# Kernel optimization log

Measured on AMD Instinct MI355X. Metric: run time of the kernel, lower is better.

The kernel has to match this reference:

```python
import jax, jax.numpy as jnp
import numpy as np

GROUPS = 32
EPS = 1e-5


def group_norm(x, gamma, beta):
    # x: [B,H,W,C], channels_last, groups over channel dim (Keras GroupNormalization default)
    B, H, W, C = x.shape
    xg = x.reshape(B, H, W, GROUPS, C // GROUPS)
    mean = xg.mean(axis=(1, 2, 4), keepdims=True)
    var = xg.var(axis=(1, 2, 4), keepdims=True)
    xn = ((xg - mean) * jax.lax.rsqrt(var + EPS)).reshape(B, H, W, C)
    return xn * gamma + beta


def conv1x1(x, w, b):
    # 1x1 conv == per-pixel dense: [B,H,W,C] x [C,D] -> [B,H,W,D]
    return jnp.einsum('bhwc,cd->bhwd', x, w) + b


def setup_inputs() -> dict:
    key = jax.random.key(0)
    ks = jax.random.split(key, 10)
    C = 512
    s = 1.0 / np.sqrt(C)
    inp = {
        'x': jax.random.normal(ks[0], (2, 64, 64, C), dtype=jnp.float32),
        'gamma': jnp.ones((C,), jnp.float32),
        'beta': jnp.zeros((C,), jnp.float32),
        'wq': jax.random.normal(ks[1], (C, C), jnp.float32) * s,
        'bq': jnp.zeros((C,), jnp.float32),
        'wk': jax.random.normal(ks[2], (C, C), jnp.float32) * s,
        'bk': jnp.zeros((C,), jnp.float32),
        'wv': jax.random.normal(ks[3], (C, C), jnp.float32) * s,
        'bv': jnp.zeros((C,), jnp.float32),
        'wp': jax.random.normal(ks[4], (C, C), jnp.float32) * s,
        'bp': jnp.zeros((C,), jnp.float32),
    }
    return inp


def reference(x, gamma, beta, wq, bq, wk, bk, wv, bv, wp, bp):
    B, H, W, C = x.shape
    N = H * W
    xn = group_norm(x, gamma, beta)
    q = conv1x1(xn, wq, bq).reshape(B, N, C)
    k = conv1x1(xn, wk, bk).reshape(B, N, C)
    v = conv1x1(xn, wv, bv).reshape(B, N, C)
    scale = 1.0 / jnp.sqrt(jnp.asarray(C, x.dtype))
    scores = jnp.einsum('bnc,bmc->bnm', q, k) * scale  # [B,N,N]
    attn = jax.nn.softmax(scores, axis=-1)
    out = jnp.einsum('bnm,bmc->bnc', attn, v).reshape(B, H, W, C)
    return conv1x1(out, wp, bp) + x
```

## Files before the change

kernel.cpp:

```cpp
#include <hip/hip_runtime.h>
#include <hip/hip_fp16.h>

typedef _Float16 half_t;
typedef _Float16 half8 __attribute__((ext_vector_type(8)));
typedef float floatx4 __attribute__((ext_vector_type(4)));

static constexpr int BATCH = 2;
static constexpr int NSP = 4096;
static constexpr int CH = 512;
static constexpr int NQKV = 3 * CH;
static constexpr int KSPLIT = 4;

static constexpr size_t OFF_STATS = 0;
static constexpr size_t OFF_ROWSUM = 512;
static constexpr size_t OFF_PST = 33280;
static constexpr size_t OFF_WQKV = 196608;
static constexpr size_t WQKV_BYTES = (size_t)NQKV * CH * 2;
static constexpr size_t OFF_WP = OFF_WQKV + WQKV_BYTES;
static constexpr size_t WP_BYTES = (size_t)CH * CH * 2;
static constexpr size_t OFF_XN = OFF_WP + WP_BYTES;
static constexpr size_t XN_BYTES = (size_t)BATCH * NSP * CH * 2;
static constexpr size_t OFF_QKV = OFF_XN + XN_BYTES;
static constexpr size_t QKV_BYTES = (size_t)BATCH * NSP * NQKV * 2;
static constexpr size_t OFF_VT = OFF_QKV + QKV_BYTES;
static constexpr size_t OFF_AO = OFF_VT + XN_BYTES;
static constexpr size_t OFF_S = OFF_AO + XN_BYTES;
static constexpr size_t S_BYTES_1 = (size_t)NSP * NSP * 2;
static constexpr size_t OFF_PART = OFF_XN;

__device__ __forceinline__ void gld16(void* lds, const void* g) {
  __builtin_amdgcn_global_load_lds(
      (__attribute__((address_space(1))) void*)(g),
      (__attribute__((address_space(3))) void*)(lds),
      16, 0, 0);
}

#define VMCNT(n) asm volatile("s_waitcnt vmcnt(" #n ")" ::: "memory")
#define LGKM0()                                         \
  do {                                                  \
    asm volatile("s_waitcnt lgkmcnt(0)" ::: "memory");  \
    __builtin_amdgcn_sched_barrier(0);                  \
  } while (0)

__global__ __launch_bounds__(256) void prep(
    const float* __restrict__ x, float* __restrict__ pst,
    const float* __restrict__ w0, const float* __restrict__ w1,
    const float* __restrict__ w2, const float* __restrict__ w3,
    half_t* __restrict__ o0, half_t* __restrict__ o1,
    half_t* __restrict__ o2, half_t* __restrict__ o3) {
  __shared__ float gs[32], gs2[32];
  __shared__ float tw[32][33];
  const int bid = (int)blockIdx.x;
  const int tid = (int)threadIdx.x;
  if (bid < 512) {
    const int b = bid >> 8;
    const int chunk = bid & 255;
    int g = ((tid * 4) & (CH - 1)) >> 4;
    const float* base = x + (long)b * NSP * CH + (long)chunk * 16 * CH + tid * 4;
    float s = 0.f, s2 = 0.f;
#pragma unroll
    for (int it = 0; it < 8; ++it) {
      floatx4 v = *(const floatx4*)(base + (long)it * 1024);
#pragma unroll
      for (int r = 0; r < 4; ++r) { s += v[r]; s2 += v[r] * v[r]; }
    }
    if (tid < 32) { gs[tid] = 0.f; gs2[tid] = 0.f; }
    __syncthreads();
    atomicAdd(&gs[g], s);
    atomicAdd(&gs2[g], s2);
    __syncthreads();
    if (tid < 32) {
      long idx = ((long)(b * 256 + chunk) * 32 + tid) * 2;
      pst[idx] = gs[tid];
      pst[idx + 1] = gs2[tid];
    }
  } else {
    const int t = bid - 512;
    const int wz = t >> 8;
    const int r = t & 255;
    const float* w; half_t* o;
    switch (wz) {
      case 0: w = w0; o = o0; break;
      case 1: w = w1; o = o1; break;
      case 2: w = w2; o = o2; break;
      default: w = w3; o = o3; break;
    }
    int d0 = (r & 15) * 32, c0 = (r >> 4) * 32;
    int tx = tid & 31, ty = tid >> 5;
#pragma unroll
    for (int i = 0; i < 4; ++i)
      tw[ty + i * 8][tx] = w[(long)(c0 + ty + i * 8) * CH + d0 + tx];
    __syncthreads();
#pragma unroll
    for (int i = 0; i < 4; ++i) {
      int d = ty + i * 8;
      o[(long)(d0 + d) * CH + c0 + tx] = (half_t)tw[tx][d];
    }
  }
}

__global__ __launch_bounds__(256) void gn_finalize(const float* __restrict__ pst,
                                                   float* __restrict__ st,
                                                   float* __restrict__ rowsum) {
  int tid = (int)threadIdx.x;
  int bg = tid & 63;
  int p = tid >> 6;
  int b = bg >> 5, g = bg & 31;
  float s = 0.f, s2 = 0.f;
  for (int j = 0; j < 64; ++j) {
    int chunk = p * 64 + j;
    long idx = ((long)(b * 256 + chunk) * 32 + g) * 2;
    s += pst[idx];
    s2 += pst[idx + 1];
  }
  __shared__ float rs[64][4], rs2[64][4];
  rs[bg][p] = s;
  rs2[bg][p] = s2;
  __syncthreads();
  if (tid < 64) {
    float ts = rs[tid][0] + rs[tid][1] + rs[tid][2] + rs[tid][3];
    float ts2 = rs2[tid][0] + rs2[tid][1] + rs2[tid][2] + rs2[tid][3];
    const float inv = 1.f / 65536.f;
    float mean = ts * inv;
    float var = ts2 * inv - mean * mean;
    st[tid * 2] = mean;
    st[tid * 2 + 1] = rsqrtf(var + 1e-5f);
  }
  floatx4* rz = (floatx4*)rowsum;
#pragma unroll
  for (int j = 0; j < 8; ++j)
    rz[tid + j * 256] = floatx4{0.f, 0.f, 0.f, 0.f};
}

__global__ __launch_bounds__(256) void gn_apply(const float* __restrict__ x,
                                                const float* __restrict__ st,
                                                const float* __restrict__ gamma,
                                                const float* __restrict__ beta,
                                                half_t* __restrict__ xn) {
  long i = ((long)blockIdx.x * 256 + threadIdx.x) * 8;
  int c = (int)(i & (CH - 1));
  int b = (int)(i >> 21);
  int g = c >> 4;
  float mean = st[((b << 5) + g) * 2];
  float rstd = st[((b << 5) + g) * 2 + 1];
  floatx4 a = *(const floatx4*)(x + i);
  floatx4 d = *(const floatx4*)(x + i + 4);
  half8 o;
#pragma unroll
  for (int r = 0; r < 4; ++r) {
    o[r]     = (half_t)((a[r] - mean) * rstd * gamma[c + r] + beta[c + r]);
    o[r + 4] = (half_t)((d[r] - mean) * rstd * gamma[c + r + 4] + beta[c + r + 4]);
  }
  *(half8*)(xn + i) = o;
}

__global__ __launch_bounds__(256) void transpose_v(const half_t* __restrict__ v,
                                                   half_t* __restrict__ vt) {
  __shared__ half_t t[32][33];
  int b = blockIdx.z;
  int d0 = blockIdx.x * 32, n0 = blockIdx.y * 32;
  int tx = threadIdx.x & 31, ty = threadIdx.x >> 5;
  const half_t* vb = v + (long)b * NSP * NQKV;
  half_t* ob = vt + (long)b * NSP * CH;
#pragma unroll
  for (int i = 0; i < 4; ++i)
    t[ty + i * 8][tx] = vb[(long)(n0 + ty + i * 8) * NQKV + d0 + tx];
  __syncthreads();
#pragma unroll
  for (int i = 0; i < 4; ++i) {
    int d = ty + i * 8;
    ob[(long)(d0 + d) * NSP + n0 + tx] = t[tx][d];
  }
}

template <int BM, int BN, int BK, int EPI, int SWZ, int KSP, typename OutT>
__global__ __launch_bounds__(256) void gemm_nt(
    const half_t* __restrict__ X, const half_t* __restrict__ Y,
    OutT* __restrict__ Co, const float* __restrict__ b0,
    const float* __restrict__ b1, const float* __restrict__ b2,
    const float* __restrict__ resid, float* __restrict__ rowsum,
    int M, int N, int K, int ldx, int ldy, int ldc,
    long xbs, long ybs, long cbs, float scale) {
  constexpr int SM = BM / 32;
  constexpr int SN = BN / 32;
  constexpr int ROWS = BM + BN;
  constexpr int CPR = BK / 8;
  constexpr int RPW = 64 / CPR;
  constexpr int ROUNDS = (ROWS * BK * 2) / 4096;
  constexpr int KSTEPS = BK / 32;
  static_assert(BM % (4 * RPW) == 0, "no As/Bs straddle within a round");
  __shared__ __align__(16) half_t Sh[ROWS * BK];

  const int zb = blockIdx.z / KSP;
  const int ks = blockIdx.z % KSP;
  int bx, by;
  if (SWZ == 1) {
    int lin = (int)(blockIdx.x + gridDim.x * blockIdx.y);
    int wmt = 256 / (int)gridDim.x;
    by = wmt * (lin >> 8) + ((lin & 255) % wmt);
    bx = (lin & 255) / wmt;
  } else if (SWZ == 2) {
    by = blockIdx.x;
    bx = blockIdx.y;
  } else {
    bx = blockIdx.x;
    by = blockIdx.y;
  }

  const half_t* Xb = X + (long)zb * xbs + (long)ks * K;
  const half_t* Yb = Y + (long)zb * ybs + (long)ks * K;
  OutT* Cb = Co + (long)blockIdx.z * cbs;

  const int m0 = by * BM;
  const int n0 = bx * BN;
  const int tid = (int)threadIdx.x;
  const int wave = tid >> 6;
  const int lane = tid & 63;
  const int quad = lane >> 4;
  const int l16 = lane & 15;
  const int wm = wave >> 1;
  const int wn = wave & 1;

  floatx4 acc[SM][SN] = {};

  const int srow = lane / CPR;
  const int schunk = lane % CPR;
  const char* Xc = (const char*)Xb;

  int soff[ROUNDS];
  int xoff[ROUNDS];
  float xinv[ROUNDS];
#pragma unroll
  for (int r = 0; r < ROUNDS; ++r) {
    int row = r * (4 * RPW) + wave * RPW + srow;
    int gchunk = schunk ^ (row & (CPR - 1));
    const char* p = (row < BM)
        ? (const char*)(Xb + (long)(m0 + row) * ldx)
        : (const char*)(Yb + (long)(n0 + row - BM) * ldy);
    soff[r] = (int)(p + gchunk * 16 - Xc);
    if (EPI == 4) {
      if (row < BM) {
        int m = m0 + row;
        int zbm = m >> 12;
        int inner = m & (NSP - 1);
        xoff[r] = zbm * (KSPLIT * NSP * CH) + inner * CH + gchunk * 8;
        xinv[r] = 1.f / rowsum[m];
      } else {
        xoff[r] = 0;
        xinv[r] = 0.f;
      }
    }
  }

  int offA[SM], offB[SN];
#pragma unroll
  for (int i = 0; i < SM; ++i) {
    int m = wm * (BM / 2) + i * 16 + l16;
    int cc = quad ^ (m & (CPR - 1));
    offA[i] = (m * BK + cc * 8) * 2;
  }
#pragma unroll
  for (int j = 0; j < SN; ++j) {
    int n = wn * (BN / 2) + j * 16 + l16;
    int cc = quad ^ (n & (CPR - 1));
    offB[j] = (BM * BK + n * BK + cc * 8) * 2;
  }

  for (int k0 = 0; k0 < K; k0 += BK) {
#pragma unroll
    for (int r = 0; r < ROUNDS; ++r) {
      int row = r * (4 * RPW) + wave * RPW + srow;
      if (EPI == 4 && row < BM) continue;
      gld16((char*)Sh + (r * 4 + wave) * 1024, Xc + (long)soff[r]);
      soff[r] += BK * 2;
    }
    if (EPI == 4) {
#pragma unroll
      for (int r = 0; r < ROUNDS; ++r) {
        int row = r * (4 * RPW) + wave * RPW + srow;
        if (row >= BM) continue;
        const half_t* pp = X + xoff[r];
        float s[8] = {};
#pragma unroll
        for (int s4 = 0; s4 < KSPLIT; ++s4) {
          half8 h = *(const half8*)(pp + (long)s4 * (NSP * (long)CH));
#pragma unroll
          for (int e = 0; e < 8; ++e) s[e] += (float)h[e];
        }
        half8 o;
#pragma unroll
        for (int e = 0; e < 8; ++e) o[e] = (half_t)(s[e] * xinv[r]);
        *(half8*)((char*)Sh + (r * 4 + wave) * 1024 + lane * 16) = o;
        xoff[r] += BK;
      }
    }
    __syncthreads();

#pragma unroll
    for (int kk = 0; kk < KSTEPS; ++kk) {
      const int kx = kk << 6;
      half8 af[SM], bf[SN];
#pragma unroll
      for (int i = 0; i < SM; ++i)
        af[i] = *(const half8*)((const char*)Sh + (offA[i] ^ kx));
#pragma unroll
      for (int j = 0; j < SN; ++j)
        bf[j] = *(const half8*)((const char*)Sh + (offB[j] ^ kx));
#pragma unroll
      for (int i = 0; i < SM; ++i)
#pragma unroll
        for (int j = 0; j < SN; ++j)
          acc[i][j] = __builtin_amdgcn_mfma_f32_16x16x32_f16(af[i], bf[j], acc[i][j], 0, 0, 0);
    }
    __syncthreads();
  }

#pragma unroll
  for (int i = 0; i < SM; ++i) {
    int gmb = m0 + wm * (BM / 2) + i * 16 + quad * 4;
#pragma unroll
    for (int j = 0; j < SN; ++j) {
      int gn = n0 + wn * (BN / 2) + j * 16 + l16;
      float bias = 0.f, sc = 1.f;
      if (EPI == 1) {
        if (gn < CH) { bias = b0[gn]; sc = scale; }
        else if (gn < 2 * CH) { bias = b1[gn - CH]; }
        else { bias = b2[gn - 2 * CH]; }
      } else if (EPI == 2 || EPI == 4) {
        bias = b0[gn];
      }
#pragma unroll
      for (int r = 0; r < 4; ++r) {
        long idx = (long)(gmb + r) * ldc + gn;
        float v = acc[i][j][r];
        if (EPI == 1) v = (v + bias) * sc;
        if (EPI == 2 || EPI == 4) v = v + bias + resid[idx];
        Cb[idx] = (OutT)v;
      }
    }
  }
}

template <int EPI, int KSP, int SW, int TT, typename OutT>
__global__ __launch_bounds__(512, 2) void gemm8p(
    const half_t* __restrict__ X, const half_t* __restrict__ Y,
    OutT* __restrict__ Co, float* __restrict__ rowsum,
    int K, int ldx, int ldy, int ldc, long xbs, long ybs, long cbs) {
  __shared__ __align__(16) char smem[131072];
  int by, bx, zb, ks;
  if (SW == 1) {
    const int lin = (int)(blockIdx.x + (blockIdx.y << 4));
    const int xcd = lin & 7;
    const int k2 = lin >> 3;
    by = (xcd & 3) * 4 + (k2 & 3);
    bx = (xcd >> 2) * 8 + (k2 >> 2);
    zb = (int)blockIdx.z / KSP;
    ks = (int)blockIdx.z % KSP;
  } else if (SW == 2) {
    const int xcd = (int)blockIdx.x & 7;
    const int s = (int)blockIdx.x >> 3;
    const int c = xcd * 2 + (s >> 4);
    by = s & 15;
    bx = c & 1;
    ks = (c >> 1) & 3;
    zb = c >> 3;
  } else if (SW == 3) {
    const int xcd = (int)blockIdx.x & 7;
    const int k2 = (int)blockIdx.x >> 3;
    by = (xcd & 3) * 4 + (k2 & 3);
    bx = ((xcd >> 2) * 4 + (k2 >> 2)) * 2;
    zb = (int)blockIdx.z;
    ks = 0;
  } else {
    by = (int)blockIdx.x;
    bx = (int)blockIdx.y;
    zb = (int)blockIdx.z / KSP;
    ks = (int)blockIdx.z % KSP;
  }
  const int m0 = by * 256;
  int n0 = bx * 256;
  const int tid = (int)threadIdx.x;
  const int w = tid >> 6;
  const int l = tid & 63;
  const int quad = l >> 4;
  const int l16 = l & 15;
  const int wm = w >> 2;
  const int wn = w & 3;

  const half_t* Xb = X + (long)zb * xbs + (long)ks * K;
  const half_t* Yb = Y + (long)zb * ybs + (long)ks * K;
  OutT* Cb = Co + ((long)(zb * KSP + ks)) * cbs;
  const char* Xc = (const char*)Xb;

  const int lr = l >> 3;
  const int gsl = (l & 7) ^ (lr & 7);
  int soff[8];
#pragma unroll
  for (int r = 0; r < 8; ++r) {
    const int R = (r * 8 + w) * 8 + lr;
    const char* p = (R < 256)
        ? (const char*)(Xb + (long)(m0 + R) * ldx)
        : (const char*)(Yb + (long)(n0 + R - 256) * ldy);
    soff[r] = (int)(p + gsl * 16 - Xc);
  }

  int offA[8], offB[4];
#pragma unroll
  for (int i = 0; i < 8; ++i) {
    const int m = wm * 128 + i * 16 + l16;
    offA[i] = m * 128 + ((quad ^ (m & 7)) << 4);
  }
#pragma unroll
  for (int j = 0; j < 4; ++j) {
    const int n = wn * 64 + j * 16 + l16;
    offB[j] = 32768 + n * 128 + ((quad ^ (n & 7)) << 4);
  }

#pragma unroll
  for (int r = 0; r < 8; ++r) {
    gld16(smem + (r * 8 + w) * 1024, Xc + (long)soff[r]);
    soff[r] += 128;
  }
  {
    constexpr int pr[6] = {4, 5, 6, 7, 0, 2};
#pragma unroll
    for (int t = 0; t < 6; ++t) {
      gld16(smem + 65536 + (pr[t] * 8 + w) * 1024, Xc + (long)soff[pr[t]]);
      soff[pr[t]] += 128;
    }
  }

  const int NI = K >> 7;
  half8 bf[4][2];

  for (int tt = 0; tt < TT; ++tt) {
    floatx4 acc[8][4] = {};
    VMCNT(6);
    __builtin_amdgcn_s_barrier();

    for (int it = 0; it < NI; ++it) {
      const bool last = (it == NI - 1);
      constexpr int sr0[8] = {1, 4, 6, 0, 1, 4, 6, 0};
      constexpr int sr1[8] = {3, 5, 7, 2, 3, 5, 7, 2};
      constexpr int spar[8] = {1, 0, 0, 0, 0, 1, 1, 1};
      constexpr int hoist[8] = {1, 1, 1, 0, 1, 0, 1, 0};
      half8 af[2][2];
#pragma unroll
      for (int ph = 0; ph < 8; ++ph) {
        const int q = ph & 3;
        const char* bb = smem + (ph >> 2) * 65536;
        if (q == 0) {
#pragma unroll
          for (int j = 0; j < 4; ++j)
#pragma unroll
            for (int kk = 0; kk < 2; ++kk)
              bf[j][kk] = *(const half8*)(bb + (offB[j] ^ (kk << 6)));
#pragma unroll
          for (int i2 = 0; i2 < 2; ++i2)
#pragma unroll
            for (int kk = 0; kk < 2; ++kk)
              af[i2][kk] = *(const half8*)(bb + (offA[i2] ^ (kk << 6)));
        } else if (ph == 6) {
#pragma unroll
          for (int i2 = 0; i2 < 2; ++i2)
#pragma unroll
            for (int kk = 0; kk < 2; ++kk)
              af[i2][kk] = *(const half8*)(bb + (offA[q * 2 + i2] ^ (kk << 6)));
        }
        if (ph == 0 || !last) {
          const int r0 = sr0[ph], r1 = sr1[ph];
          char* db = smem + spar[ph] * 65536;
          gld16(db + (r0 * 8 + w) * 1024, Xc + (long)soff[r0]);
          soff[r0] += 128;
          gld16(db + (r1 * 8 + w) * 1024, Xc + (long)soff[r1]);
          soff[r1] += 128;
        }
        LGKM0();
        __builtin_amdgcn_s_setprio(1);
#pragma unroll
        for (int i2 = 0; i2 < 2; ++i2)
#pragma unroll
          for (int j = 0; j < 4; ++j)
#pragma unroll
            for (int kk = 0; kk < 2; ++kk)
              acc[q * 2 + i2][j] = __builtin_amdgcn_mfma_f32_16x16x32_f16(
                  af[i2][kk], bf[j][kk], acc[q * 2 + i2][j], 0, 0, 0);
        __builtin_amdgcn_s_setprio(0);
        if (ph == 3) {
          if (last) { VMCNT(2); } else { VMCNT(8); }
        } else if (ph == 5) {
          if (last) { VMCNT(0); } else { VMCNT(10); }
        }
        if (hoist[ph]) {
          const int np = ph + 1;
          const int nq = np & 3;
          const char* nb = smem + ((np >> 2) & 1) * 65536;
#pragma unroll
          for (int i2 = 0; i2 < 2; ++i2)
#pragma unroll
            for (int kk = 0; kk < 2; ++kk)
              af[i2][kk] = *(const half8*)(nb + (offA[nq * 2 + i2] ^ (kk << 6)));
          __builtin_amdgcn_sched_barrier(0);
        }
        if (ph == 7) {
          if (!last) { VMCNT(6); }
        }
        __builtin_amdgcn_s_barrier();
      }
    }

    if (TT == 2 && tt == 0) {
      const int n1 = n0 + 256;
#pragma unroll
      for (int r = 0; r < 8; ++r) {
        const int R = (r * 8 + w) * 8 + lr;
        const char* p = (R < 256)
            ? (const char*)(Xb + (long)(m0 + R) * ldx)
            : (const char*)(Yb + (long)(n1 + R - 256) * ldy);
        soff[r] = (int)(p + gsl * 16 - Xc);
      }
#pragma unroll
      for (int r = 0; r < 8; ++r) {
        gld16(smem + (r * 8 + w) * 1024, Xc + (long)soff[r]);
        soff[r] += 128;
      }
      constexpr int pr[6] = {4, 5, 6, 7, 0, 2};
#pragma unroll
      for (int t = 0; t < 6; ++t) {
        gld16(smem + 65536 + (pr[t] * 8 + w) * 1024, Xc + (long)soff[pr[t]]);
        soff[pr[t]] += 128;
      }
    }

#pragma unroll
    for (int i = 0; i < 8; ++i) {
      const int gmb = m0 + wm * 128 + i * 16 + quad * 4;
      float rs[4] = {0.f, 0.f, 0.f, 0.f};
#pragma unroll
      for (int j = 0; j < 4; ++j) {
        const int gn = n0 + wn * 64 + j * 16 + l16;
#pragma unroll
        for (int r = 0; r < 4; ++r) {
          long idx = (long)(gmb + r) * ldc + gn;
          float v = acc[i][j][r];
          if (EPI == 3) { v = __expf(v); rs[r] += v; }
          Cb[idx] = (OutT)v;
        }
      }
      if (EPI == 3) {
#pragma unroll
        for (int r = 0; r < 4; ++r) {
          float v = rs[r];
          v += __shfl_xor(v, 1);
          v += __shfl_xor(v, 2);
          v += __shfl_xor(v, 4);
          v += __shfl_xor(v, 8);
          if (l16 == 0) atomicAdd(&rowsum[(long)zb * NSP + gmb + r], v);
        }
      }
    }
    n0 += 256;
  }
}

__global__ __launch_bounds__(256) void pv_combine(const half_t* __restrict__ part,
                                                  const float* __restrict__ rowsum,
                                                  half_t* __restrict__ ao) {
  const long bNC = (long)NSP * CH;
  long i = ((long)blockIdx.x * 256 + threadIdx.x) * 8;
  int b = (int)(i >> 21);
  long inner = i & ((1L << 21) - 1);
  float inv = 1.f / rowsum[i >> 9];
  float s[8] = {};
#pragma unroll
  for (int ks = 0; ks < KSPLIT; ++ks) {
    half8 h = *(const half8*)(part + ((long)(b * KSPLIT + ks)) * bNC + inner);
#pragma unroll
    for (int r = 0; r < 8; ++r) s[r] += (float)h[r];
  }
  half8 o;
#pragma unroll
  for (int r = 0; r < 8; ++r) o[r] = (half_t)(s[r] * inv);
  *(half8*)(ao + i) = o;
}

extern "C" void kernel_launch(void* const* d_in, const int* in_sizes, int n_in,
                              void* d_out, int out_size, void* d_ws, size_t ws_size,
                              hipStream_t stream) {
  const float* x = (const float*)d_in[0];
  const float* gamma = (const float*)d_in[1];
  const float* beta = (const float*)d_in[2];
  const float* wq = (const float*)d_in[3];
  const float* bq = (const float*)d_in[4];
  const float* wk = (const float*)d_in[5];
  const float* bk = (const float*)d_in[6];
  const float* wv = (const float*)d_in[7];
  const float* bv = (const float*)d_in[8];
  const float* wp = (const float*)d_in[9];
  const float* bp = (const float*)d_in[10];
  float* out = (float*)d_out;
  char* ws = (char*)d_ws;

  float* st = (float*)(ws + OFF_STATS);
  float* rsum = (float*)(ws + OFF_ROWSUM);
  float* pst = (float*)(ws + OFF_PST);
  half_t* wqkvT = (half_t*)(ws + OFF_WQKV);
  half_t* wpT = (half_t*)(ws + OFF_WP);
  half_t* xn = (half_t*)(ws + OFF_XN);
  half_t* qkv = (half_t*)(ws + OFF_QKV);
  half_t* vt = (half_t*)(ws + OFF_VT);
  half_t* ao = (half_t*)(ws + OFF_AO);
  half_t* S = (half_t*)(ws + OFF_S);
  half_t* part = (half_t*)(ws + OFF_PART);

  half_t* q = qkv;
  half_t* k = qkv + CH;
  half_t* v = qkv + 2 * CH;

  const float scale = 0.044194173824159216f;
  const long bQKV = (long)NSP * NQKV;
  const long bNC = (long)NSP * CH;
  const long bNN = (long)NSP * NSP;

  prep<<<1536, 256, 0, stream>>>(x, pst, wq, wk, wv, wp,
      wqkvT, wqkvT + (size_t)CH * CH, wqkvT + 2 * (size_t)CH * CH, wpT);
  gn_finalize<<<1, 256, 0, stream>>>(pst, st, rsum);
  gn_apply<<<2048, 256, 0, stream>>>(x, st, gamma, beta, xn);

  gemm_nt<128, 128, 64, 1, 2, 1, half_t><<<dim3(BATCH * NSP / 128, NQKV / 128, 1), 256, 0, stream>>>(
      xn, wqkvT, qkv, bq, bk, bv, nullptr, nullptr, BATCH * NSP, NQKV, CH,
      CH, CH, NQKV, 0, 0, 0, scale);
  transpose_v<<<dim3(16, 128, BATCH), 256, 0, stream>>>(v, vt);

  bool full = ws_size >= OFF_S + 2 * S_BYTES_1;
  if (full) {
    gemm8p<3, 1, 1, 1, half_t><<<dim3(16, 16, BATCH), 512, 0, stream>>>(
        q, k, S, rsum, CH, NQKV, NQKV, NSP, bQKV, bQKV, bNN);
    gemm8p<0, KSPLIT, 2, 1, half_t><<<dim3(256, 1, 1), 512, 0, stream>>>(
        S, vt, part, nullptr, NSP / KSPLIT, NSP, NSP, CH, bNN, bNC, bNC);
    gemm_nt<64, 64, 128, 4, 2, 1, float><<<dim3(BATCH * NSP / 64, CH / 64, 1), 256, 0, stream>>>(
        part, wpT, out, bp, nullptr, nullptr, x, rsum, BATCH * NSP, CH, CH,
        CH, CH, CH, 0, 0, 0, 1.f);
  } else {
    for (int bb = 0; bb < BATCH; ++bb) {
      gemm8p<3, 1, 1, 1, half_t><<<dim3(16, 16, 1), 512, 0, stream>>>(
          q + bb * bQKV, k + bb * bQKV, S, rsum + bb * NSP, CH,
          NQKV, NQKV, NSP, 0, 0, 0);
      gemm8p<0, KSPLIT, 0, 1, half_t><<<dim3(NSP / 256, CH / 256, KSPLIT), 512, 0, stream>>>(
          S, vt + bb * bNC, part + (long)bb * KSPLIT * bNC, nullptr,
          NSP / KSPLIT, NSP, NSP, CH, 0, 0, bNC);
    }
    pv_combine<<<2048, 256, 0, stream>>>(part, rsum, ao);
    gemm_nt<64, 64, 128, 2, 2, 1, float><<<dim3(BATCH * NSP / 64, CH / 64, 1), 256, 0, stream>>>(
        ao, wpT, out, bp, nullptr, nullptr, x, nullptr, BATCH * NSP, CH, CH,
        CH, CH, CH, 0, 0, 0, 1.f);
  }
}
```

Measured before the change: 234.3 us.

## Fuse group-norm apply and V transpose into the QKV projection GEMM

Adds an EPI==5 mode to gemm_nt that reads fp32 x directly, applies the group-norm mean/rstd with gamma/beta while staging the A tile into LDS, and for V-column tiles writes the result transposed through LDS straight into vt. This removes the gn_apply and transpose_v launches and the xn round trip through global memory in the full-workspace path. In exchange, the GEMM prologue now issues synchronous fp32 loads plus normalization math per k-step instead of async fp16 copies, which may stall the MMA loop. Unused SW==3 and TT==2 code paths in gemm8p are also deleted.

Result: slower. 251.4 us (+7.3%).

```diff
diff --git a/kernel.cpp b/kernel.cpp
--- a/kernel.cpp
+++ b/kernel.cpp
@@ -179,6 +179,9 @@
     OutT* __restrict__ Co, const float* __restrict__ b0,
     const float* __restrict__ b1, const float* __restrict__ b2,
     const float* __restrict__ resid, float* __restrict__ rowsum,
+    const float* __restrict__ xf, const float* __restrict__ stv,
+    const float* __restrict__ gma, const float* __restrict__ bta,
+    half_t* __restrict__ vtp,
     int M, int N, int K, int ldx, int ldy, int ldc,
     long xbs, long ybs, long cbs, float scale) {
   constexpr int SM = BM / 32;
@@ -250,6 +253,24 @@
         xinv[r] = 0.f;
       }
     }
+    if (EPI == 5) {
+      if (row < BM) {
+        int m = m0 + row;
+        xoff[r] = (m >> 12) * (NSP * CH) + (m & (NSP - 1)) * CH + gchunk * 8;
+      } else {
+        xoff[r] = 0;
+      }
+    }
+  }
+  int xg8[ROUNDS], xb32[ROUNDS];
+  if (EPI == 5) {
+#pragma unroll
+    for (int r = 0; r < ROUNDS; ++r) {
+      int row = r * (4 * RPW) + wave * RPW + srow;
+      int gchunk = schunk ^ (row & (CPR - 1));
+      xg8[r] = gchunk * 8;
+      xb32[r] = ((m0 + row) >> 12) * 32;
+    }
   }
 
   int offA[SM], offB[SN];
@@ -270,7 +291,7 @@
 #pragma unroll
     for (int r = 0; r < ROUNDS; ++r) {
       int row = r * (4 * RPW) + wave * RPW + srow;
-      if (EPI == 4 && row < BM) continue;
+      if ((EPI == 4 || EPI == 5) && row < BM) continue;
       gld16((char*)Sh + (r * 4 + wave) * 1024, Xc + (long)soff[r]);
       soff[r] += BK * 2;
     }
@@ -294,6 +315,31 @@
         xoff[r] += BK;
       }
     }
+    if (EPI == 5) {
+#pragma unroll
+      for (int r = 0; r < ROUNDS; ++r) {
+        int row = r * (4 * RPW) + wave * RPW + srow;
+        if (row >= BM) continue;
+        const float* xp = xf + xoff[r] + k0;
+        floatx4 a0 = *(const floatx4*)xp;
+        floatx4 a1 = *(const floatx4*)(xp + 4);
+        int c = k0 + xg8[r];
+        int g = c >> 4;
+        float mean = stv[(xb32[r] + g) * 2];
+        float rstd = stv[(xb32[r] + g) * 2 + 1];
+        floatx4 g0 = *(const floatx4*)(gma + c);
+        floatx4 g1 = *(const floatx4*)(gma + c + 4);
+        floatx4 be0 = *(const floatx4*)(bta + c);
+        floatx4 be1 = *(const floatx4*)(bta + c + 4);
+        half8 o;
+#pragma unroll
+        for (int e = 0; e < 4; ++e) {
+          o[e]     = (half_t)((a0[e] - mean) * rstd * g0[e] + be0[e]);
+          o[e + 4] = (half_t)((a1[e] - mean) * rstd * g1[e] + be1[e]);
+        }
+        *(half8*)((char*)Sh + (r * 4 + wave) * 1024 + lane * 16) = o;
+      }
+    }
     __syncthreads();
 
 #pragma unroll
@@ -315,27 +361,67 @@
     __syncthreads();
   }
 
-#pragma unroll
-  for (int i = 0; i < SM; ++i) {
-    int gmb = m0 + wm * (BM / 2) + i * 16 + quad * 4;
-#pragma unroll
-    for (int j = 0; j < SN; ++j) {
-      int gn = n0 + wn * (BN / 2) + j * 16 + l16;
-      float bias = 0.f, sc = 1.f;
-      if (EPI == 1) {
-        if (gn < CH) { bias = b0[gn]; sc = scale; }
-        else if (gn < 2 * CH) { bias = b1[gn - CH]; }
-        else { bias = b2[gn - 2 * CH]; }
-      } else if (EPI == 2 || EPI == 4) {
-        bias = b0[gn];
-      }
-#pragma unroll
-      for (int r = 0; r < 4; ++r) {
-        long idx = (long)(gmb + r) * ldc + gn;
-        float v = acc[i][j][r];
-        if (EPI == 1) v = (v + bias) * sc;
-        if (EPI == 2 || EPI == 4) v = v + bias + resid[idx];
-        Cb[idx] = (OutT)v;
+  if (EPI == 5 && n0 >= 2 * CH) {
+    half_t* lds = (half_t*)Sh;
+    half_t* vtb = vtp + (long)(m0 >> 12) * NSP * CH;
+    const int mi = m0 & (NSP - 1);
+    const int d0 = n0 - 2 * CH;
+#pragma unroll
+    for (int p = 0; p < 2; ++p) {
+      if (p) __syncthreads();
+      if (wn == p) {
+#pragma unroll
+        for (int i = 0; i < SM; ++i) {
+          int mloc = wm * 64 + i * 16 + quad * 4;
+#pragma unroll
+          for (int j = 0; j < SN; ++j) {
+            int nl = j * 16 + l16;
+            float bias = b2[d0 + p * 64 + nl];
+#pragma unroll
+            for (int r = 0; r < 4; ++r)
+              lds[nl * 130 + mloc + r] = (half_t)(acc[i][j][r] + bias);
+          }
+        }
+      }
+      __syncthreads();
+#pragma unroll
+      for (int h = 0; h < 2; ++h) {
+        int dloc = (tid >> 3) + h * 32;
+        int mseg = (tid & 7) * 16;
+        half8 o0, o1;
+#pragma unroll
+        for (int e = 0; e < 8; ++e) {
+          o0[e] = lds[dloc * 130 + mseg + e];
+          o1[e] = lds[dloc * 130 + mseg + 8 + e];
+        }
+        long vrow = (long)(d0 + p * 64 + dloc) * NSP + mi + mseg;
+        *(half8*)(vtb + vrow) = o0;
+        *(half8*)(vtb + vrow + 8) = o1;
+      }
+    }
+  } else {
+#pragma unroll
+    for (int i = 0; i < SM; ++i) {
+      int gmb = m0 + wm * (BM / 2) + i * 16 + quad * 4;
+#pragma unroll
+      for (int j = 0; j < SN; ++j) {
+        int gn = n0 + wn * (BN / 2) + j * 16 + l16;
+        float bias = 0.f, sc = 1.f;
+        if (EPI == 1 || EPI == 5) {
+          if (gn < CH) { bias = b0[gn]; sc = scale; }
+          else if (gn < 2 * CH) { bias = b1[gn - CH]; }
+          else { bias = b2[gn - 2 * CH]; }
+        } else if (EPI == 2 || EPI == 4) {
+          bias = b0[gn];
+        }
+#pragma unroll
+        for (int r = 0; r < 4; ++r) {
+          long idx = (long)(gmb + r) * ldc + gn;
+          float v = acc[i][j][r];
+          if (EPI == 1 || EPI == 5) v = (v + bias) * sc;
+          if (EPI == 2 || EPI == 4) v = v + bias + resid[idx];
+          Cb[idx] = (OutT)v;
+        }
       }
     }
   }
@@ -364,13 +450,6 @@
     bx = c & 1;
     ks = (c >> 1) & 3;
     zb = c >> 3;
-  } else if (SW == 3) {
-    const int xcd = (int)blockIdx.x & 7;
-    const int k2 = (int)blockIdx.x >> 3;
-    by = (xcd & 3) * 4 + (k2 & 3);
-    bx = ((xcd >> 2) * 4 + (k2 >> 2)) * 2;
-    zb = (int)blockIdx.z;
-    ks = 0;
   } else {
     by = (int)blockIdx.x;
     bx = (int)blockIdx.y;
@@ -506,29 +585,6 @@
           if (!last) { VMCNT(6); }
         }
         __builtin_amdgcn_s_barrier();
-      }
-    }
-
-    if (TT == 2 && tt == 0) {
-      const int n1 = n0 + 256;
-#pragma unroll
-      for (int r = 0; r < 8; ++r) {
-        const int R = (r * 8 + w) * 8 + lr;
-        const char* p = (R < 256)
-            ? (const char*)(Xb + (long)(m0 + R) * ldx)
-            : (const char*)(Yb + (long)(n1 + R - 256) * ldy);
-        soff[r] = (int)(p + gsl * 16 - Xc);
-      }
-#pragma unroll
-      for (int r = 0; r < 8; ++r) {
-        gld16(smem + (r * 8 + w) * 1024, Xc + (long)soff[r]);
-        soff[r] += 128;
-      }
-      constexpr int pr[6] = {4, 5, 6, 7, 0, 2};
-#pragma unroll
-      for (int t = 0; t < 6; ++t) {
-        gld16(smem + 65536 + (pr[t] * 8 + w) * 1024, Xc + (long)soff[pr[t]]);
-        soff[pr[t]] += 128;
       }
     }
 
@@ -625,23 +681,28 @@
   prep<<<1536, 256, 0, stream>>>(x, pst, wq, wk, wv, wp,
       wqkvT, wqkvT + (size_t)CH * CH, wqkvT + 2 * (size_t)CH * CH, wpT);
   gn_finalize<<<1, 256, 0, stream>>>(pst, st, rsum);
-  gn_apply<<<2048, 256, 0, stream>>>(x, st, gamma, beta, xn);
-
-  gemm_nt<128, 128, 64, 1, 2, 1, half_t><<<dim3(BATCH * NSP / 128, NQKV / 128, 1), 256, 0, stream>>>(
-      xn, wqkvT, qkv, bq, bk, bv, nullptr, nullptr, BATCH * NSP, NQKV, CH,
-      CH, CH, NQKV, 0, 0, 0, scale);
-  transpose_v<<<dim3(16, 128, BATCH), 256, 0, stream>>>(v, vt);
 
   bool full = ws_size >= OFF_S + 2 * S_BYTES_1;
   if (full) {
+    gemm_nt<128, 128, 64, 5, 2, 1, half_t><<<dim3(BATCH * NSP / 128, NQKV / 128, 1), 256, 0, stream>>>(
+        wqkvT, wqkvT, qkv, bq, bk, bv, nullptr, nullptr,
+        x, st, gamma, beta, vt,
+        BATCH * NSP, NQKV, CH, CH, CH, NQKV, 0, 0, 0, scale);
     gemm8p<3, 1, 1, 1, half_t><<<dim3(16, 16, BATCH), 512, 0, stream>>>(
         q, k, S, rsum, CH, NQKV, NQKV, NSP, bQKV, bQKV, bNN);
     gemm8p<0, KSPLIT, 2, 1, half_t><<<dim3(256, 1, 1), 512, 0, stream>>>(
         S, vt, part, nullptr, NSP / KSPLIT, NSP, NSP, CH, bNN, bNC, bNC);
     gemm_nt<64, 64, 128, 4, 2, 1, float><<<dim3(BATCH * NSP / 64, CH / 64, 1), 256, 0, stream>>>(
-        part, wpT, out, bp, nullptr, nullptr, x, rsum, BATCH * NSP, CH, CH,
-        CH, CH, CH, 0, 0, 0, 1.f);
+        part, wpT, out, bp, nullptr, nullptr, x, rsum,
+        nullptr, nullptr, nullptr, nullptr, nullptr,
+        BATCH * NSP, CH, CH, CH, CH, CH, 0, 0, 0, 1.f);
   } else {
+    gn_apply<<<2048, 256, 0, stream>>>(x, st, gamma, beta, xn);
+    gemm_nt<128, 128, 64, 1, 2, 1, half_t><<<dim3(BATCH * NSP / 128, NQKV / 128, 1), 256, 0, stream>>>(
+        xn, wqkvT, qkv, bq, bk, bv, nullptr, nullptr,
+        nullptr, nullptr, nullptr, nullptr, nullptr,
+        BATCH * NSP, NQKV, CH, CH, CH, NQKV, 0, 0, 0, scale);
+    transpose_v<<<dim3(16, 128, BATCH), 256, 0, stream>>>(v, vt);
     for (int bb = 0; bb < BATCH; ++bb) {
       gemm8p<3, 1, 1, 1, half_t><<<dim3(16, 16, 1), 512, 0, stream>>>(
           q + bb * bQKV, k + bb * bQKV, S, rsum + bb * NSP, CH,
@@ -652,7 +713,8 @@
     }
     pv_combine<<<2048, 256, 0, stream>>>(part, rsum, ao);
     gemm_nt<64, 64, 128, 2, 2, 1, float><<<dim3(BATCH * NSP / 64, CH / 64, 1), 256, 0, stream>>>(
-        ao, wpT, out, bp, nullptr, nullptr, x, nullptr, BATCH * NSP, CH, CH,
-        CH, CH, CH, 0, 0, 0, 1.f);
-  }
-}
+        ao, wpT, out, bp, nullptr, nullptr, x, nullptr,
+        nullptr, nullptr, nullptr, nullptr, nullptr,
+        BATCH * NSP, CH, CH, CH, CH, CH, 0, 0, 0, 1.f);
+  }
+}
```
